# Performance work log

Measured on AMD Instinct MI355X. Metric: run time of the kernel, lower is better.

The kernel has to match this reference:

```python
import jax, jax.numpy as jnp
import numpy as np

B, H, W, C = 4, 256, 256, 128
HEADS, WS, SHIFT = 4, 8, 4
EPS = 1e-5


def _rel_pos_index(ws):
    coords = np.stack(np.meshgrid(np.arange(ws), np.arange(ws), indexing='ij'))
    cf = coords.reshape(2, -1)
    rel = (cf[:, :, None] - cf[:, None, :]).transpose(1, 2, 0)
    rel[:, :, 0] += ws - 1
    rel[:, :, 1] += ws - 1
    rel[:, :, 0] *= 2 * ws - 1
    return rel.sum(-1).reshape(-1)

REL_IDX = jnp.array(_rel_pos_index(WS))


def _shift_mask(h, w, ws, shift):
    img = np.zeros((1, h, w, 1))
    cnt = 0
    sl = (slice(0, -ws), slice(-ws, -shift), slice(-shift, None))
    for hs in sl:
        for wsl in sl:
            img[:, hs, wsl, :] = cnt
            cnt += 1
    m = img.reshape(1, h // ws, ws, w // ws, ws, 1).transpose(0, 1, 3, 2, 4, 5).reshape(-1, ws * ws)
    am = m[:, None, :] - m[:, :, None]
    return jnp.array(np.where(am != 0, -100.0, 0.0).astype(np.float32))

ATTN_MASK = _shift_mask(H, W, WS, SHIFT)  # (nW, ws*ws, ws*ws)


def _ln(x, scale, bias):
    mu = x.mean(-1, keepdims=True)
    var = x.var(-1, keepdims=True)
    return (x - mu) / jnp.sqrt(var + EPS) * scale + bias


def setup_inputs() -> dict:
    key = jax.random.key(0)
    ks = jax.random.split(key, 8)
    s = 0.02
    return dict(
        hidden_states=jax.random.normal(ks[0], (B, H * W, C), jnp.float32),
        ln1_scale=jnp.ones((C,), jnp.float32), ln1_bias=jnp.zeros((C,), jnp.float32),
        q_w=jax.random.normal(ks[1], (C, C), jnp.float32) * s, q_b=jnp.zeros((C,), jnp.float32),
        k_w=jax.random.normal(ks[2], (C, C), jnp.float32) * s, k_b=jnp.zeros((C,), jnp.float32),
        v_w=jax.random.normal(ks[3], (C, C), jnp.float32) * s, v_b=jnp.zeros((C,), jnp.float32),
        proj_w=jax.random.normal(ks[4], (C, C), jnp.float32) * s, proj_b=jnp.zeros((C,), jnp.float32),
        rpb_table=jax.random.normal(ks[5], ((2 * WS - 1) ** 2, HEADS), jnp.float32) * s,
        ln2_scale=jnp.ones((C,), jnp.float32), ln2_bias=jnp.zeros((C,), jnp.float32),
        fc1_w=jax.random.normal(ks[6], (C, 4 * C), jnp.float32) * s, fc1_b=jnp.zeros((4 * C,), jnp.float32),
        fc2_w=jax.random.normal(ks[7], (4 * C, C), jnp.float32) * s, fc2_b=jnp.zeros((C,), jnp.float32),
    )


def reference(hidden_states, ln1_scale, ln1_bias, q_w, q_b, k_w, k_b, v_w, v_b,
              proj_w, proj_b, rpb_table, ln2_scale, ln2_bias, fc1_w, fc1_b, fc2_w, fc2_b):
    hd = C // HEADS
    T = WS * WS
    nW = (H // WS) * (W // WS)
    shortcut = hidden_states
    x = _ln(hidden_states, ln1_scale, ln1_bias).reshape(B, H, W, C)
    # cyclic shift
    x = jnp.roll(x, (-SHIFT, -SHIFT), axis=(1, 2))
    # window partition -> (B*nW, T, C)
    x = x.reshape(B, H // WS, WS, W // WS, WS, C).transpose(0, 1, 3, 2, 4, 5).reshape(-1, T, C)
    q = (x @ q_w + q_b).reshape(-1, T, HEADS, hd) / jnp.sqrt(jnp.float32(hd))
    k = (x @ k_w + k_b).reshape(-1, T, HEADS, hd)
    v = (x @ v_w + v_b).reshape(-1, T, HEADS, hd)
    attn = jnp.einsum('bqhd,bkhd->bhqk', q, k)
    bias = rpb_table[REL_IDX].reshape(T, T, HEADS).transpose(2, 0, 1)  # (h, q, k)
    attn = attn + bias[None]
    # shift mask per window
    attn = attn.reshape(B, nW, HEADS, T, T) + ATTN_MASK[None, :, None]
    attn = jax.nn.softmax(attn.reshape(-1, HEADS, T, T), axis=-1)
    out = jnp.einsum('bhqk,bkhd->bqhd', attn, v).reshape(-1, T, C)
    out = out @ proj_w + proj_b
    # window reverse + un-shift
    out = out.reshape(B, H // WS, W // WS, WS, WS, C).transpose(0, 1, 3, 2, 4, 5).reshape(B, H, W, C)
    out = jnp.roll(out, (SHIFT, SHIFT), axis=(1, 2)).reshape(B, H * W, C)
    x = shortcut + out
    y = _ln(x, ln2_scale, ln2_bias)
    y = jax.nn.gelu(y @ fc1_w + fc1_b, approximate=False) @ fc2_w + fc2_b
    return x + y
```

## Files before the change

### kernel.cpp

```cpp
#include <hip/hip_runtime.h>
#include <hip/hip_bf16.h>
#include <math.h>

#define B_ 4
#define H_ 256
#define W_ 256
#define C_ 128
#define HEADS_ 4
#define HD_ 32
#define WS_ 8
#define SHIFT_ 4
#define T_ 64
#define NW_ 1024
#define M_ (B_*NW_*T_)

typedef float floatx4 __attribute__((ext_vector_type(4)));
typedef short bf16x8 __attribute__((ext_vector_type(8)));
typedef unsigned short ushort8v __attribute__((ext_vector_type(8)));

#define MFMA16(a,b,c) __builtin_amdgcn_mfma_f32_16x16x32_bf16(a,b,c,0,0,0)

__device__ __forceinline__ unsigned short f2b(float f){
    union { float f; unsigned int i; } c; c.f = f;
    unsigned int r = c.i + 0x7FFFu + ((c.i >> 16) & 1u);
    return (unsigned short)(r >> 16);
}
__device__ __forceinline__ int region_id(int x){ return (x < 248) ? 0 : ((x < 252) ? 1 : 2); }

__device__ __forceinline__ bf16x8 ldfrag(const unsigned short* p){
    return *(const bf16x8*)p;
}
__device__ __forceinline__ bf16x8 ldfrag_strided(const unsigned short* p, int stride){
    ushort8v u;
    #pragma unroll
    for (int j = 0; j < 8; j++) u[j] = p[j*stride];
    return __builtin_bit_cast(bf16x8, u);
}
__device__ __forceinline__ floatx4 fzero(){ floatx4 v = {0.f,0.f,0.f,0.f}; return v; }

#define WSO_QT   0
#define WSO_KT   16384
#define WSO_VT   32768
#define WSO_PT   49152
#define WSO_W1T  65536
#define WSO_W2T  131072
#define WSO_BIAS 196608
#define WS_BYTES_NEEDED (196608u*2u + 16384u*4u)

__global__ __launch_bounds__(256) void prep_weights_kernel(
        const float* __restrict__ qw, const float* __restrict__ kw,
        const float* __restrict__ vw, const float* __restrict__ pw,
        const float* __restrict__ fc1, const float* __restrict__ fc2,
        const float* __restrict__ rpb, unsigned short* __restrict__ ws)
{
    int tid = blockIdx.x * 256 + threadIdx.x;
    int nt = gridDim.x * 256;
    for (int i = tid; i < 16384; i += nt) {
        int n = i >> 7, k = i & 127;
        ws[WSO_QT + i] = f2b(qw[k*128 + n]);
        ws[WSO_KT + i] = f2b(kw[k*128 + n]);
        ws[WSO_VT + i] = f2b(vw[k*128 + n]);
        ws[WSO_PT + i] = f2b(pw[k*128 + n]);
    }
    for (int i = tid; i < 65536; i += nt) {
        int n = i >> 7, k = i & 127;
        ws[WSO_W1T + i] = f2b(fc1[(size_t)k*512 + n]);
    }
    for (int i = tid; i < 65536; i += nt) {
        int n = i >> 9, k = i & 511;
        ws[WSO_W2T + i] = f2b(fc2[(size_t)k*128 + n]);
    }
    float* bt = (float*)(ws + WSO_BIAS);
    for (int i = tid; i < 16384; i += nt) {
        int h = i >> 12, q = (i >> 6) & 63, k = i & 63;
        int th = q >> 3, tw = q & 7, jh = k >> 3, jw = k & 7;
        bt[i] = rpb[((th - jh + 7)*15 + (tw - jw + 7))*HEADS_ + h];
    }
}

__device__ __forceinline__ void gemm64x128_g(
        const unsigned short (*Xs)[136], const unsigned short* __restrict__ Wt,
        int wv, int quad, int l15, floatx4 acc[4][2])
{
    #pragma unroll
    for (int c = 0; c < 4; c++) {
        bf16x8 bf0 = ldfrag(Wt + (size_t)(32*wv + l15)*128      + c*32 + quad*8);
        bf16x8 bf1 = ldfrag(Wt + (size_t)(32*wv + 16 + l15)*128 + c*32 + quad*8);
        #pragma unroll
        for (int m = 0; m < 4; m++) {
            bf16x8 af = ldfrag(&Xs[16*m + l15][c*32 + quad*8]);
            acc[m][0] = MFMA16(af, bf0, acc[m][0]);
            acc[m][1] = MFMA16(af, bf1, acc[m][1]);
        }
    }
}

__global__ __launch_bounds__(256) void swin_attn_kernel2(
        const float* __restrict__ hidden,
        const float* __restrict__ ln1_s, const float* __restrict__ ln1_b,
        const float* __restrict__ q_b, const float* __restrict__ k_b,
        const float* __restrict__ v_b, const float* __restrict__ p_b,
        const unsigned short* __restrict__ wsu,
        float* __restrict__ xres)
{
    __shared__ __align__(16) unsigned short Xs[T_][136];
    __shared__ __align__(16) unsigned short Ks[T_][136];
    __shared__ __align__(16) unsigned short Vs[T_][134];
    __shared__ __align__(16) unsigned short PhU[2][2560];

    int tid = threadIdx.x;
    int wv = tid >> 6, lane = tid & 63;
    int quad = lane >> 4, l15 = lane & 15;
    int gw = blockIdx.x;
    int wi = gw & (NW_-1), b = gw >> 10;
    int hb = wi >> 5, wb = wi & 31;

    for (int it = 0; it < 16; it++) {
        int t = wv*16 + it;
        int th = t >> 3, tw = t & 7;
        int h = (hb*8 + th + SHIFT_) & 255;
        int w = (wb*8 + tw + SHIFT_) & 255;
        size_t src = ((size_t)((b<<16) + (h<<8) + w)) * C_;
        float2 u = *(const float2*)(hidden + src + 2*lane);
        float x0 = u.x, x1 = u.y;
        float s = x0 + x1, ss = x0*x0 + x1*x1;
        #pragma unroll
        for (int m = 32; m > 0; m >>= 1) {
            s  += __shfl_xor(s,  m, 64);
            ss += __shfl_xor(ss, m, 64);
        }
        float mean = s * (1.0f/C_);
        float var  = ss * (1.0f/C_) - mean*mean;
        float rstd = rsqrtf(var + 1e-5f);
        int c0 = 2*lane;
        ushort2 o;
        o.x = f2b((x0 - mean) * rstd * ln1_s[c0]   + ln1_b[c0]);
        o.y = f2b((x1 - mean) * rstd * ln1_s[c0+1] + ln1_b[c0+1]);
        *(ushort2*)&Xs[t][c0] = o;
    }
    __syncthreads();

    {
        floatx4 acc[4][2];
        #pragma unroll
        for (int m = 0; m < 4; m++) { acc[m][0] = fzero(); acc[m][1] = fzero(); }
        gemm64x128_g(Xs, wsu + WSO_KT, wv, quad, l15, acc);
        float kb0 = k_b[32*wv + l15], kb1 = k_b[32*wv + 16 + l15];
        #pragma unroll
        for (int m = 0; m < 4; m++)
            #pragma unroll
            for (int r = 0; r < 4; r++) {
                int q = 16*m + 4*quad + r;
                Ks[q][32*wv + l15]      = f2b(acc[m][0][r] + kb0);
                Ks[q][32*wv + 16 + l15] = f2b(acc[m][1][r] + kb1);
            }
    }
    {
        floatx4 acc[4][2];
        #pragma unroll
        for (int m = 0; m < 4; m++) { acc[m][0] = fzero(); acc[m][1] = fzero(); }
        gemm64x128_g(Xs, wsu + WSO_VT, wv, quad, l15, acc);
        float vb0 = v_b[32*wv + l15], vb1 = v_b[32*wv + 16 + l15];
        #pragma unroll
        for (int m = 0; m < 4; m++)
            #pragma unroll
            for (int r = 0; r < 4; r++) {
                int q = 16*m + 4*quad + r;
                Vs[q][32*wv + l15]      = f2b(acc[m][0][r] + vb0);
                Vs[q][32*wv + 16 + l15] = f2b(acc[m][1][r] + vb1);
            }
    }
    floatx4 qacc[4][2];
    #pragma unroll
    for (int m = 0; m < 4; m++) { qacc[m][0] = fzero(); qacc[m][1] = fzero(); }
    gemm64x128_g(Xs, wsu + WSO_QT, wv, quad, l15, qacc);
    __syncthreads();
    {
        const float sc = 0.17677669529663687f;
        float qb0 = q_b[32*wv + l15], qb1 = q_b[32*wv + 16 + l15];
        #pragma unroll
        for (int m = 0; m < 4; m++)
            #pragma unroll
            for (int r = 0; r < 4; r++) {
                int q = 16*m + 4*quad + r;
                Xs[q][32*wv + l15]      = f2b((qacc[m][0][r] + qb0) * sc);
                Xs[q][32*wv + 16 + l15] = f2b((qacc[m][1][r] + qb1) * sc);
            }
    }

    floatx4 sacc[4][4];
    #pragma unroll
    for (int m = 0; m < 4; m++)
        #pragma unroll
        for (int n = 0; n < 4; n++) sacc[m][n] = fzero();
    {
        bf16x8 qf[4], kf[4];
        #pragma unroll
        for (int m = 0; m < 4; m++) qf[m] = ldfrag(&Xs[16*m + l15][32*wv + quad*8]);
        #pragma unroll
        for (int n = 0; n < 4; n++) kf[n] = ldfrag(&Ks[16*n + l15][32*wv + quad*8]);
        #pragma unroll
        for (int m = 0; m < 4; m++)
            #pragma unroll
            for (int n = 0; n < 4; n++) sacc[m][n] = MFMA16(qf[m], kf[n], sacc[m][n]);
    }
    __syncthreads();

    {
        const float* bt = (const float*)(wsu + WSO_BIAS) + (wv << 12);
        int cidj_[4];
        #pragma unroll
        for (int n = 0; n < 4; n++) {
            int kt = 16*n + l15;
            cidj_[n] = region_id(hb*8 + (kt >> 3))*3 + region_id(wb*8 + (kt & 7));
        }
        #pragma unroll
        for (int m = 0; m < 4; m++)
            #pragma unroll
            for (int r = 0; r < 4; r++) {
                int q = 16*m + 4*quad + r;
                int cidi = region_id(hb*8 + (q >> 3))*3 + region_id(wb*8 + (q & 7));
                float v[4];
                #pragma unroll
                for (int n = 0; n < 4; n++) {
                    float d = sacc[m][n][r] + bt[q*64 + 16*n + l15];
                    if (cidi != cidj_[n]) d -= 100.f;
                    v[n] = d;
                }
                float mx = fmaxf(fmaxf(v[0],v[1]), fmaxf(v[2],v[3]));
                #pragma unroll
                for (int off = 1; off < 16; off <<= 1) mx = fmaxf(mx, __shfl_xor(mx, off, 64));
                float sum = 0.f;
                #pragma unroll
                for (int n = 0; n < 4; n++) { v[n] = __expf(v[n] - mx); sum += v[n]; }
                #pragma unroll
                for (int off = 1; off < 16; off <<= 1) sum += __shfl_xor(sum, off, 64);
                float inv = 1.0f / sum;
                #pragma unroll
                for (int n = 0; n < 4; n++) sacc[m][n][r] = v[n] * inv;
            }
    }

    unsigned short* Ph = (wv < 2) ? (&Ks[0][0] + wv*2560) : &PhU[wv-2][0];
    floatx4 oacc[4][2];
    #pragma unroll
    for (int m = 0; m < 4; m++) { oacc[m][0] = fzero(); oacc[m][1] = fzero(); }
    for (int kb = 0; kb < 2; kb++) {
        #pragma unroll
        for (int m = 0; m < 4; m++)
            #pragma unroll
            for (int r = 0; r < 4; r++) {
                int q = 16*m + 4*quad + r;
                Ph[q*40 + l15]      = f2b(sacc[m][2*kb+0][r]);
                Ph[q*40 + 16 + l15] = f2b(sacc[m][2*kb+1][r]);
            }
        bf16x8 bf0 = ldfrag_strided(&Vs[kb*32 + quad*8][32*wv + l15],      134);
        bf16x8 bf1 = ldfrag_strided(&Vs[kb*32 + quad*8][32*wv + 16 + l15], 134);
        #pragma unroll
        for (int m = 0; m < 4; m++) {
            bf16x8 af = ldfrag(&Ph[(16*m + l15)*40 + quad*8]);
            oacc[m][0] = MFMA16(af, bf0, oacc[m][0]);
            oacc[m][1] = MFMA16(af, bf1, oacc[m][1]);
        }
    }
    #pragma unroll
    for (int m = 0; m < 4; m++)
        #pragma unroll
        for (int r = 0; r < 4; r++) {
            int q = 16*m + 4*quad + r;
            Xs[q][32*wv + l15]      = f2b(oacc[m][0][r]);
            Xs[q][32*wv + 16 + l15] = f2b(oacc[m][1][r]);
        }
    __syncthreads();
    {
        floatx4 acc[4][2];
        #pragma unroll
        for (int m = 0; m < 4; m++) { acc[m][0] = fzero(); acc[m][1] = fzero(); }
        gemm64x128_g(Xs, wsu + WSO_PT, wv, quad, l15, acc);
        float pb0 = p_b[32*wv + l15], pb1 = p_b[32*wv + 16 + l15];
        #pragma unroll
        for (int m = 0; m < 4; m++)
            #pragma unroll
            for (int r = 0; r < 4; r++) {
                int t = 16*m + 4*quad + r;
                int th = t >> 3, tw = t & 7;
                int h = (hb*8 + th + SHIFT_) & 255;
                int w = (wb*8 + tw + SHIFT_) & 255;
                size_t dst = ((size_t)((b<<16) + (h<<8) + w)) * C_;
                int c0 = 32*wv + l15;
                xres[dst + c0]      = hidden[dst + c0]      + acc[m][0][r] + pb0;
                xres[dst + c0 + 16] = hidden[dst + c0 + 16] + acc[m][1][r] + pb1;
            }
    }
}

__global__ __launch_bounds__(256) void mlp_ln_kernel2(
        float* __restrict__ xio,
        const float* __restrict__ ln2_s, const float* __restrict__ ln2_b,
        const float* __restrict__ b1, const float* __restrict__ b2,
        const unsigned short* __restrict__ wsu)
{
    __shared__ __align__(16) unsigned short As[T_][136];
    __shared__ __align__(16) unsigned short G[T_][72];
    const unsigned short* W1t = wsu + WSO_W1T;
    const unsigned short* W2t = wsu + WSO_W2T;
    int tid = threadIdx.x, wv = tid >> 6, lane = tid & 63;
    int quad = lane >> 4, l15 = lane & 15;
    size_t row0 = (size_t)blockIdx.x * 64;

    for (int it = 0; it < 16; it++) {
        int t = wv*16 + it;
        const float* xp = xio + (row0 + t)*C_;
        float2 u = *(const float2*)(xp + 2*lane);
        float x0 = u.x, x1 = u.y;
        float s = x0 + x1, ss = x0*x0 + x1*x1;
        #pragma unroll
        for (int m = 32; m > 0; m >>= 1) {
            s  += __shfl_xor(s,  m, 64);
            ss += __shfl_xor(ss, m, 64);
        }
        float mean = s * (1.0f/C_);
        float var  = ss * (1.0f/C_) - mean*mean;
        float rstd = rsqrtf(var + 1e-5f);
        int c0 = 2*lane;
        ushort2 o;
        o.x = f2b((x0 - mean) * rstd * ln2_s[c0]   + ln2_b[c0]);
        o.y = f2b((x1 - mean) * rstd * ln2_s[c0+1] + ln2_b[c0+1]);
        *(ushort2*)&As[t][c0] = o;
    }
    __syncthreads();

    floatx4 acc2[4][2];
    #pragma unroll
    for (int m = 0; m < 4; m++) { acc2[m][0] = fzero(); acc2[m][1] = fzero(); }

    for (int ch = 0; ch < 8; ch++) {
        floatx4 a1[4];
        #pragma unroll
        for (int m = 0; m < 4; m++) a1[m] = fzero();
        #pragma unroll
        for (int kc = 0; kc < 4; kc++) {
            bf16x8 bfrag = ldfrag(W1t + (size_t)(ch*64 + 16*wv + l15)*128 + kc*32 + quad*8);
            #pragma unroll
            for (int m = 0; m < 4; m++) {
                bf16x8 af = ldfrag(&As[16*m + l15][kc*32 + quad*8]);
                a1[m] = MFMA16(af, bfrag, a1[m]);
            }
        }
        __syncthreads();
        {
            int c_rel = 16*wv + l15;
            float bb = b1[ch*64 + c_rel];
            #pragma unroll
            for (int m = 0; m < 4; m++)
                #pragma unroll
                for (int r = 0; r < 4; r++) {
                    int q = 16*m + 4*quad + r;
                    float hh = a1[m][r] + bb;
                    float g = 0.5f * hh * (1.0f + erff(hh * 0.70710678118654752f));
                    G[q][c_rel] = f2b(g);
                }
        }
        __syncthreads();
        #pragma unroll
        for (int ki = 0; ki < 2; ki++) {
            bf16x8 bf0 = ldfrag(W2t + (size_t)(32*wv + l15)*512      + ch*64 + ki*32 + quad*8);
            bf16x8 bf1 = ldfrag(W2t + (size_t)(32*wv + 16 + l15)*512 + ch*64 + ki*32 + quad*8);
            #pragma unroll
            for (int m = 0; m < 4; m++) {
                bf16x8 af = ldfrag(&G[16*m + l15][ki*32 + quad*8]);
                acc2[m][0] = MFMA16(af, bf0, acc2[m][0]);
                acc2[m][1] = MFMA16(af, bf1, acc2[m][1]);
            }
        }
    }
    {
        float bb0 = b2[32*wv + l15], bb1 = b2[32*wv + 16 + l15];
        #pragma unroll
        for (int m = 0; m < 4; m++)
            #pragma unroll
            for (int r = 0; r < 4; r++) {
                size_t rr = row0 + 16*m + 4*quad + r;
                int c0 = 32*wv + l15;
                xio[rr*C_ + c0]      += acc2[m][0][r] + bb0;
                xio[rr*C_ + c0 + 16] += acc2[m][1][r] + bb1;
            }
    }
}


__device__ __forceinline__ void gemm64x128(
        const unsigned short (*Xs)[136], unsigned short (*Wc)[132],
        const float* __restrict__ Wg, int tid, int wv, int quad, int l15,
        floatx4 acc[4][2])
{
    for (int c = 0; c < 4; c++) {
        __syncthreads();
        #pragma unroll
        for (int it = 0; it < 4; it++) {
            int idx = tid + it*256;
            int kk = idx >> 5;
            int n4 = (idx & 31) * 4;
            float4 v = *(const float4*)(Wg + (size_t)(c*32 + kk)*C_ + n4);
            ushort4 o; o.x=f2b(v.x); o.y=f2b(v.y); o.z=f2b(v.z); o.w=f2b(v.w);
            *(ushort4*)&Wc[kk][n4] = o;
        }
        __syncthreads();
        bf16x8 bf0 = ldfrag_strided(&Wc[quad*8][32*wv + l15],      132);
        bf16x8 bf1 = ldfrag_strided(&Wc[quad*8][32*wv + 16 + l15], 132);
        #pragma unroll
        for (int m = 0; m < 4; m++) {
            bf16x8 af = ldfrag(&Xs[16*m + l15][c*32 + quad*8]);
            acc[m][0] = MFMA16(af, bf0, acc[m][0]);
            acc[m][1] = MFMA16(af, bf1, acc[m][1]);
        }
    }
}

__global__ __launch_bounds__(256) void swin_attn_kernel(
        const float* __restrict__ hidden,
        const float* __restrict__ ln1_s, const float* __restrict__ ln1_b,
        const float* __restrict__ q_w, const float* __restrict__ q_b,
        const float* __restrict__ k_w, const float* __restrict__ k_b,
        const float* __restrict__ v_w, const float* __restrict__ v_b,
        const float* __restrict__ p_w, const float* __restrict__ p_b,
        const float* __restrict__ rpb,
        float* __restrict__ xres)
{
    __shared__ unsigned short Xs[T_][136];
    __shared__ unsigned short Ks[T_][136];
    __shared__ unsigned short Vs[T_][134];
    __shared__ __align__(16) unsigned char U[10240];

    unsigned short (*Wc)[132] = (unsigned short(*)[132])U;
    float* rpbf = (float*)U;

    int tid = threadIdx.x;
    int wv = tid >> 6, lane = tid & 63;
    int quad = lane >> 4, l15 = lane & 15;
    int gw = blockIdx.x;
    int wi = gw & (NW_-1), b = gw >> 10;
    int hb = wi >> 5, wb = wi & 31;

    for (int it = 0; it < 16; it++) {
        int t = wv*16 + it;
        int th = t >> 3, tw = t & 7;
        int h = (hb*8 + th + SHIFT_) & 255;
        int w = (wb*8 + tw + SHIFT_) & 255;
        size_t src = ((size_t)((b<<16) + (h<<8) + w)) * C_;
        float2 u = *(const float2*)(hidden + src + 2*lane);
        float x0 = u.x, x1 = u.y;
        float s = x0 + x1, ss = x0*x0 + x1*x1;
        #pragma unroll
        for (int m = 32; m > 0; m >>= 1) {
            s  += __shfl_xor(s,  m, 64);
            ss += __shfl_xor(ss, m, 64);
        }
        float mean = s * (1.0f/C_);
        float var  = ss * (1.0f/C_) - mean*mean;
        float rstd = rsqrtf(var + 1e-5f);
        int c0 = 2*lane;
        ushort2 o;
        o.x = f2b((x0 - mean) * rstd * ln1_s[c0]   + ln1_b[c0]);
        o.y = f2b((x1 - mean) * rstd * ln1_s[c0+1] + ln1_b[c0+1]);
        *(ushort2*)&Xs[t][c0] = o;
    }

    {
        floatx4 acc[4][2];
        #pragma unroll
        for (int m = 0; m < 4; m++) { acc[m][0] = fzero(); acc[m][1] = fzero(); }
        gemm64x128(Xs, Wc, k_w, tid, wv, quad, l15, acc);
        float kb0 = k_b[32*wv + l15], kb1 = k_b[32*wv + 16 + l15];
        #pragma unroll
        for (int m = 0; m < 4; m++)
            #pragma unroll
            for (int r = 0; r < 4; r++) {
                int q = 16*m + 4*quad + r;
                Ks[q][32*wv + l15]      = f2b(acc[m][0][r] + kb0);
                Ks[q][32*wv + 16 + l15] = f2b(acc[m][1][r] + kb1);
            }
    }
    {
        floatx4 acc[4][2];
        #pragma unroll
        for (int m = 0; m < 4; m++) { acc[m][0] = fzero(); acc[m][1] = fzero(); }
        gemm64x128(Xs, Wc, v_w, tid, wv, quad, l15, acc);
        float vb0 = v_b[32*wv + l15], vb1 = v_b[32*wv + 16 + l15];
        #pragma unroll
        for (int m = 0; m < 4; m++)
            #pragma unroll
            for (int r = 0; r < 4; r++) {
                int q = 16*m + 4*quad + r;
                Vs[q][32*wv + l15]      = f2b(acc[m][0][r] + vb0);
                Vs[q][32*wv + 16 + l15] = f2b(acc[m][1][r] + vb1);
            }
    }
    floatx4 qacc[4][2];
    #pragma unroll
    for (int m = 0; m < 4; m++) { qacc[m][0] = fzero(); qacc[m][1] = fzero(); }
    gemm64x128(Xs, Wc, q_w, tid, wv, quad, l15, qacc);
    __syncthreads();
    for (int i = tid; i < 225*HEADS_; i += 256) rpbf[i] = rpb[i];
    {
        const float sc = 0.17677669529663687f;
        float qb0 = q_b[32*wv + l15], qb1 = q_b[32*wv + 16 + l15];
        #pragma unroll
        for (int m = 0; m < 4; m++)
            #pragma unroll
            for (int r = 0; r < 4; r++) {
                int q = 16*m + 4*quad + r;
                Xs[q][32*wv + l15]      = f2b((qacc[m][0][r] + qb0) * sc);
                Xs[q][32*wv + 16 + l15] = f2b((qacc[m][1][r] + qb1) * sc);
            }
    }
    __syncthreads();

    floatx4 sacc[4][4];
    #pragma unroll
    for (int m = 0; m < 4; m++)
        #pragma unroll
        for (int n = 0; n < 4; n++) sacc[m][n] = fzero();
    {
        bf16x8 qf[4], kf[4];
        #pragma unroll
        for (int m = 0; m < 4; m++) qf[m] = ldfrag(&Xs[16*m + l15][32*wv + quad*8]);
        #pragma unroll
        for (int n = 0; n < 4; n++) kf[n] = ldfrag(&Ks[16*n + l15][32*wv + quad*8]);
        #pragma unroll
        for (int m = 0; m < 4; m++)
            #pragma unroll
            for (int n = 0; n < 4; n++) sacc[m][n] = MFMA16(qf[m], kf[n], sacc[m][n]);
    }
    {
        int jh_[4], jw_[4], cidj_[4];
        #pragma unroll
        for (int n = 0; n < 4; n++) {
            int kt = 16*n + l15;
            jh_[n] = kt >> 3; jw_[n] = kt & 7;
            cidj_[n] = region_id(hb*8 + jh_[n])*3 + region_id(wb*8 + jw_[n]);
        }
        #pragma unroll
        for (int m = 0; m < 4; m++)
            #pragma unroll
            for (int r = 0; r < 4; r++) {
                int q = 16*m + 4*quad + r;
                int th = q >> 3, twq = q & 7;
                int cidi = region_id(hb*8 + th)*3 + region_id(wb*8 + twq);
                float v[4];
                #pragma unroll
                for (int n = 0; n < 4; n++) {
                    float d = sacc[m][n][r];
                    d += rpbf[((th - jh_[n] + 7)*15 + (twq - jw_[n] + 7))*HEADS_ + wv];
                    if (cidi != cidj_[n]) d -= 100.f;
                    v[n] = d;
                }
                float mx = fmaxf(fmaxf(v[0],v[1]), fmaxf(v[2],v[3]));
                #pragma unroll
                for (int off = 1; off < 16; off <<= 1) mx = fmaxf(mx, __shfl_xor(mx, off, 64));
                float sum = 0.f;
                #pragma unroll
                for (int n = 0; n < 4; n++) { v[n] = __expf(v[n] - mx); sum += v[n]; }
                #pragma unroll
                for (int off = 1; off < 16; off <<= 1) sum += __shfl_xor(sum, off, 64);
                float inv = 1.0f / sum;
                #pragma unroll
                for (int n = 0; n < 4; n++) sacc[m][n][r] = v[n] * inv;
            }
    }
    __syncthreads();

    unsigned short* Ph = (wv < 2) ? (&Ks[0][0] + wv*2560)
                                  : ((unsigned short*)U + (wv-2)*2560);
    floatx4 oacc[4][2];
    #pragma unroll
    for (int m = 0; m < 4; m++) { oacc[m][0] = fzero(); oacc[m][1] = fzero(); }
    for (int kb = 0; kb < 2; kb++) {
        #pragma unroll
        for (int m = 0; m < 4; m++)
            #pragma unroll
            for (int r = 0; r < 4; r++) {
                int q = 16*m + 4*quad + r;
                Ph[q*40 + l15]      = f2b(sacc[m][2*kb+0][r]);
                Ph[q*40 + 16 + l15] = f2b(sacc[m][2*kb+1][r]);
            }
        __syncthreads();
        bf16x8 bf0 = ldfrag_strided(&Vs[kb*32 + quad*8][32*wv + l15],      134);
        bf16x8 bf1 = ldfrag_strided(&Vs[kb*32 + quad*8][32*wv + 16 + l15], 134);
        #pragma unroll
        for (int m = 0; m < 4; m++) {
            bf16x8 af = ldfrag(&Ph[(16*m + l15)*40 + quad*8]);
            oacc[m][0] = MFMA16(af, bf0, oacc[m][0]);
            oacc[m][1] = MFMA16(af, bf1, oacc[m][1]);
        }
        __syncthreads();
    }
    #pragma unroll
    for (int m = 0; m < 4; m++)
        #pragma unroll
        for (int r = 0; r < 4; r++) {
            int q = 16*m + 4*quad + r;
            Xs[q][32*wv + l15]      = f2b(oacc[m][0][r]);
            Xs[q][32*wv + 16 + l15] = f2b(oacc[m][1][r]);
        }
    {
        floatx4 acc[4][2];
        #pragma unroll
        for (int m = 0; m < 4; m++) { acc[m][0] = fzero(); acc[m][1] = fzero(); }
        gemm64x128(Xs, Wc, p_w, tid, wv, quad, l15, acc);
        float pb0 = p_b[32*wv + l15], pb1 = p_b[32*wv + 16 + l15];
        #pragma unroll
        for (int m = 0; m < 4; m++)
            #pragma unroll
            for (int r = 0; r < 4; r++) {
                int t = 16*m + 4*quad + r;
                int th = t >> 3, tw = t & 7;
                int h = (hb*8 + th + SHIFT_) & 255;
                int w = (wb*8 + tw + SHIFT_) & 255;
                size_t dst = ((size_t)((b<<16) + (h<<8) + w)) * C_;
                int c0 = 32*wv + l15;
                xres[dst + c0]      = hidden[dst + c0]      + acc[m][0][r] + pb0;
                xres[dst + c0 + 16] = hidden[dst + c0 + 16] + acc[m][1][r] + pb1;
            }
    }
}

__global__ __launch_bounds__(256) void mlp_ln_kernel(
        float* __restrict__ xio,
        const float* __restrict__ ln2_s, const float* __restrict__ ln2_b,
        const float* __restrict__ W1, const float* __restrict__ b1,
        const float* __restrict__ W2, const float* __restrict__ b2)
{
    __shared__ unsigned short As[T_][136];
    __shared__ unsigned short G[T_][72];
    __shared__ unsigned short W1c[C_][68];
    __shared__ unsigned short W2c[T_][132];
    int tid = threadIdx.x, wv = tid >> 6, lane = tid & 63;
    int quad = lane >> 4, l15 = lane & 15;
    size_t row0 = (size_t)blockIdx.x * 64;

    for (int it = 0; it < 16; it++) {
        int t = wv*16 + it;
        const float* xp = xio + (row0 + t)*C_;
        float2 u = *(const float2*)(xp + 2*lane);
        float x0 = u.x, x1 = u.y;
        float s = x0 + x1, ss = x0*x0 + x1*x1;
        #pragma unroll
        for (int m = 32; m > 0; m >>= 1) {
            s  += __shfl_xor(s,  m, 64);
            ss += __shfl_xor(ss, m, 64);
        }
        float mean = s * (1.0f/C_);
        float var  = ss * (1.0f/C_) - mean*mean;
        float rstd = rsqrtf(var + 1e-5f);
        int c0 = 2*lane;
        ushort2 o;
        o.x = f2b((x0 - mean) * rstd * ln2_s[c0]   + ln2_b[c0]);
        o.y = f2b((x1 - mean) * rstd * ln2_s[c0+1] + ln2_b[c0+1]);
        *(ushort2*)&As[t][c0] = o;
    }

    floatx4 acc2[4][2];
    #pragma unroll
    for (int m = 0; m < 4; m++) { acc2[m][0] = fzero(); acc2[m][1] = fzero(); }

    for (int ch = 0; ch < 8; ch++) {
        __syncthreads();
        #pragma unroll
        for (int it = 0; it < 8; it++) {
            int idx = tid + it*256;
            int k = idx >> 4, n4 = (idx & 15) * 4;
            float4 v = *(const float4*)(W1 + (size_t)k*512 + ch*64 + n4);
            ushort4 o; o.x=f2b(v.x); o.y=f2b(v.y); o.z=f2b(v.z); o.w=f2b(v.w);
            *(ushort4*)&W1c[k][n4] = o;
        }
        #pragma unroll
        for (int it = 0; it < 8; it++) {
            int idx = tid + it*256;
            int k = idx >> 5, n4 = (idx & 31) * 4;
            float4 v = *(const float4*)(W2 + (size_t)(ch*64 + k)*C_ + n4);
            ushort4 o; o.x=f2b(v.x); o.y=f2b(v.y); o.z=f2b(v.z); o.w=f2b(v.w);
            *(ushort4*)&W2c[k][n4] = o;
        }
        __syncthreads();
        floatx4 a1[4];
        #pragma unroll
        for (int m = 0; m < 4; m++) a1[m] = fzero();
        #pragma unroll
        for (int kc = 0; kc < 4; kc++) {
            bf16x8 bfrag = ldfrag_strided(&W1c[kc*32 + quad*8][16*wv + l15], 68);
            #pragma unroll
            for (int m = 0; m < 4; m++) {
                bf16x8 af = ldfrag(&As[16*m + l15][kc*32 + quad*8]);
                a1[m] = MFMA16(af, bfrag, a1[m]);
            }
        }
        {
            int c_rel = 16*wv + l15;
            float bb = b1[ch*64 + c_rel];
            #pragma unroll
            for (int m = 0; m < 4; m++)
                #pragma unroll
                for (int r = 0; r < 4; r++) {
                    int q = 16*m + 4*quad + r;
                    float hh = a1[m][r] + bb;
                    float g = 0.5f * hh * (1.0f + erff(hh * 0.70710678118654752f));
                    G[q][c_rel] = f2b(g);
                }
        }
        __syncthreads();
        #pragma unroll
        for (int ki = 0; ki < 2; ki++) {
            bf16x8 bf0 = ldfrag_strided(&W2c[ki*32 + quad*8][32*wv + l15],      132);
            bf16x8 bf1 = ldfrag_strided(&W2c[ki*32 + quad*8][32*wv + 16 + l15], 132);
            #pragma unroll
            for (int m = 0; m < 4; m++) {
                bf16x8 af = ldfrag(&G[16*m + l15][ki*32 + quad*8]);
                acc2[m][0] = MFMA16(af, bf0, acc2[m][0]);
                acc2[m][1] = MFMA16(af, bf1, acc2[m][1]);
            }
        }
    }
    {
        float bb0 = b2[32*wv + l15], bb1 = b2[32*wv + 16 + l15];
        #pragma unroll
        for (int m = 0; m < 4; m++)
            #pragma unroll
            for (int r = 0; r < 4; r++) {
                size_t rr = row0 + 16*m + 4*quad + r;
                int c0 = 32*wv + l15;
                xio[rr*C_ + c0]      += acc2[m][0][r] + bb0;
                xio[rr*C_ + c0 + 16] += acc2[m][1][r] + bb1;
            }
    }
}

extern "C" void kernel_launch(void* const* d_in, const int* in_sizes, int n_in,
                              void* d_out, int out_size, void* d_ws, size_t ws_size,
                              hipStream_t stream) {
    (void)in_sizes; (void)n_in; (void)out_size;
    const float* hidden = (const float*)d_in[0];
    const float* ln1_s  = (const float*)d_in[1];
    const float* ln1_b  = (const float*)d_in[2];
    const float* q_w    = (const float*)d_in[3];
    const float* q_b    = (const float*)d_in[4];
    const float* k_w    = (const float*)d_in[5];
    const float* k_b    = (const float*)d_in[6];
    const float* v_w    = (const float*)d_in[7];
    const float* v_b    = (const float*)d_in[8];
    const float* p_w    = (const float*)d_in[9];
    const float* p_b    = (const float*)d_in[10];
    const float* rpb    = (const float*)d_in[11];
    const float* ln2_s  = (const float*)d_in[12];
    const float* ln2_b  = (const float*)d_in[13];
    const float* fc1_w  = (const float*)d_in[14];
    const float* fc1_b  = (const float*)d_in[15];
    const float* fc2_w  = (const float*)d_in[16];
    const float* fc2_b  = (const float*)d_in[17];
    float* outp = (float*)d_out;

    if (d_ws != nullptr && ws_size >= (size_t)WS_BYTES_NEEDED) {
        unsigned short* wsu = (unsigned short*)d_ws;
        prep_weights_kernel<<<64, 256, 0, stream>>>(q_w, k_w, v_w, p_w,
                fc1_w, fc2_w, rpb, wsu);
        swin_attn_kernel2<<<B_*NW_, 256, 0, stream>>>(hidden, ln1_s, ln1_b,
                q_b, k_b, v_b, p_b, wsu, outp);
        mlp_ln_kernel2<<<M_/64, 256, 0, stream>>>(outp, ln2_s, ln2_b,
                fc1_b, fc2_b, wsu);
    } else {
        swin_attn_kernel<<<B_*NW_, 256, 0, stream>>>(hidden, ln1_s, ln1_b,
                q_w, q_b, k_w, k_b, v_w, v_b, p_w, p_b, rpb, outp);
        mlp_ln_kernel<<<M_/64, 256, 0, stream>>>(outp, ln2_s, ln2_b,
                fc1_w, fc1_b, fc2_w, fc2_b);
    }
}
```

Before: 560.3 us.

## Restructure MLP per-wave rows, fuse K/V GEMMs, transpose score layout

```diff
diff --git a/kernel.cpp b/kernel.cpp
--- a/kernel.cpp
+++ b/kernel.cpp
@@ -106,7 +106,6 @@
     __shared__ __align__(16) unsigned short Xs[T_][136];
     __shared__ __align__(16) unsigned short Ks[T_][136];
     __shared__ __align__(16) unsigned short Vs[T_][134];
-    __shared__ __align__(16) unsigned short PhU[2][2560];
 
     int tid = threadIdx.x;
     int wv = tid >> 6, lane = tid & 63;
@@ -115,59 +114,76 @@
     int wi = gw & (NW_-1), b = gw >> 10;
     int hb = wi >> 5, wb = wi & 31;
 
-    for (int it = 0; it < 16; it++) {
-        int t = wv*16 + it;
+    {
+        int rloc = lane >> 2;
+        int t = wv*16 + rloc;
         int th = t >> 3, tw = t & 7;
         int h = (hb*8 + th + SHIFT_) & 255;
         int w = (wb*8 + tw + SHIFT_) & 255;
-        size_t src = ((size_t)((b<<16) + (h<<8) + w)) * C_;
-        float2 u = *(const float2*)(hidden + src + 2*lane);
-        float x0 = u.x, x1 = u.y;
-        float s = x0 + x1, ss = x0*x0 + x1*x1;
-        #pragma unroll
-        for (int m = 32; m > 0; m >>= 1) {
-            s  += __shfl_xor(s,  m, 64);
-            ss += __shfl_xor(ss, m, 64);
-        }
+        int c0 = (lane & 3) * 32;
+        const float* xp = hidden + ((size_t)((b<<16) + (h<<8) + w)) * C_ + c0;
+        float4 xv[8];
+        float s = 0.f, ss = 0.f;
+        #pragma unroll
+        for (int i = 0; i < 8; i++) {
+            xv[i] = *((const float4*)xp + i);
+            s  += xv[i].x + xv[i].y + xv[i].z + xv[i].w;
+            ss += xv[i].x*xv[i].x + xv[i].y*xv[i].y + xv[i].z*xv[i].z + xv[i].w*xv[i].w;
+        }
+        s  += __shfl_xor(s, 1, 64);  s  += __shfl_xor(s, 2, 64);
+        ss += __shfl_xor(ss, 1, 64); ss += __shfl_xor(ss, 2, 64);
         float mean = s * (1.0f/C_);
         float var  = ss * (1.0f/C_) - mean*mean;
         float rstd = rsqrtf(var + 1e-5f);
-        int c0 = 2*lane;
-        ushort2 o;
-        o.x = f2b((x0 - mean) * rstd * ln1_s[c0]   + ln1_b[c0]);
-        o.y = f2b((x1 - mean) * rstd * ln1_s[c0+1] + ln1_b[c0+1]);
-        *(ushort2*)&Xs[t][c0] = o;
+        #pragma unroll
+        for (int i = 0; i < 8; i++) {
+            float4 sc = *((const float4*)(ln1_s + c0) + i);
+            float4 bi = *((const float4*)(ln1_b + c0) + i);
+            ushort4 o;
+            o.x = f2b((xv[i].x - mean)*rstd*sc.x + bi.x);
+            o.y = f2b((xv[i].y - mean)*rstd*sc.y + bi.y);
+            o.z = f2b((xv[i].z - mean)*rstd*sc.z + bi.z);
+            o.w = f2b((xv[i].w - mean)*rstd*sc.w + bi.w);
+            *(ushort4*)&Xs[t][c0 + 4*i] = o;
+        }
     }
     __syncthreads();
 
     {
-        floatx4 acc[4][2];
-        #pragma unroll
-        for (int m = 0; m < 4; m++) { acc[m][0] = fzero(); acc[m][1] = fzero(); }
-        gemm64x128_g(Xs, wsu + WSO_KT, wv, quad, l15, acc);
+        floatx4 kacc[4][2], vacc[4][2];
+        #pragma unroll
+        for (int m = 0; m < 4; m++) {
+            kacc[m][0] = fzero(); kacc[m][1] = fzero();
+            vacc[m][0] = fzero(); vacc[m][1] = fzero();
+        }
+        const unsigned short* Kt = wsu + WSO_KT;
+        const unsigned short* Vt = wsu + WSO_VT;
+        #pragma unroll
+        for (int c = 0; c < 4; c++) {
+            size_t off0 = (size_t)(32*wv + l15)*128      + c*32 + quad*8;
+            size_t off1 = (size_t)(32*wv + 16 + l15)*128 + c*32 + quad*8;
+            bf16x8 kb0 = ldfrag(Kt + off0), kb1 = ldfrag(Kt + off1);
+            bf16x8 vb0 = ldfrag(Vt + off0), vb1 = ldfrag(Vt + off1);
+            #pragma unroll
+            for (int m = 0; m < 4; m++) {
+                bf16x8 af = ldfrag(&Xs[16*m + l15][c*32 + quad*8]);
+                kacc[m][0] = MFMA16(af, kb0, kacc[m][0]);
+                kacc[m][1] = MFMA16(af, kb1, kacc[m][1]);
+                vacc[m][0] = MFMA16(af, vb0, vacc[m][0]);
+                vacc[m][1] = MFMA16(af, vb1, vacc[m][1]);
+            }
+        }
         float kb0 = k_b[32*wv + l15], kb1 = k_b[32*wv + 16 + l15];
+        float vb0 = v_b[32*wv + l15], vb1 = v_b[32*wv + 16 + l15];
         #pragma unroll
         for (int m = 0; m < 4; m++)
             #pragma unroll
             for (int r = 0; r < 4; r++) {
                 int q = 16*m + 4*quad + r;
-                Ks[q][32*wv + l15]      = f2b(acc[m][0][r] + kb0);
-                Ks[q][32*wv + 16 + l15] = f2b(acc[m][1][r] + kb1);
-            }
-    }
-    {
-        floatx4 acc[4][2];
-        #pragma unroll
-        for (int m = 0; m < 4; m++) { acc[m][0] = fzero(); acc[m][1] = fzero(); }
-        gemm64x128_g(Xs, wsu + WSO_VT, wv, quad, l15, acc);
-        float vb0 = v_b[32*wv + l15], vb1 = v_b[32*wv + 16 + l15];
-        #pragma unroll
-        for (int m = 0; m < 4; m++)
-            #pragma unroll
-            for (int r = 0; r < 4; r++) {
-                int q = 16*m + 4*quad + r;
-                Vs[q][32*wv + l15]      = f2b(acc[m][0][r] + vb0);
-                Vs[q][32*wv + 16 + l15] = f2b(acc[m][1][r] + vb1);
+                Ks[q][32*wv + l15]      = f2b(kacc[m][0][r] + kb0);
+                Ks[q][32*wv + 16 + l15] = f2b(kacc[m][1][r] + kb1);
+                Vs[q][32*wv + l15]      = f2b(vacc[m][0][r] + vb0);
+                Vs[q][32*wv + 16 + l15] = f2b(vacc[m][1][r] + vb1);
             }
     }
     floatx4 qacc[4][2];
@@ -202,46 +218,55 @@
         #pragma unroll
         for (int m = 0; m < 4; m++)
             #pragma unroll
-            for (int n = 0; n < 4; n++) sacc[m][n] = MFMA16(qf[m], kf[n], sacc[m][n]);
+            for (int n = 0; n < 4; n++) sacc[m][n] = MFMA16(kf[n], qf[m], sacc[m][n]);
     }
     __syncthreads();
 
     {
         const float* bt = (const float*)(wsu + WSO_BIAS) + (wv << 12);
-        int cidj_[4];
-        #pragma unroll
-        for (int n = 0; n < 4; n++) {
-            int kt = 16*n + l15;
-            cidj_[n] = region_id(hb*8 + (kt >> 3))*3 + region_id(wb*8 + (kt & 7));
-        }
-        #pragma unroll
-        for (int m = 0; m < 4; m++)
-            #pragma unroll
-            for (int r = 0; r < 4; r++) {
-                int q = 16*m + 4*quad + r;
-                int cidi = region_id(hb*8 + (q >> 3))*3 + region_id(wb*8 + (q & 7));
-                float v[4];
-                #pragma unroll
-                for (int n = 0; n < 4; n++) {
-                    float d = sacc[m][n][r] + bt[q*64 + 16*n + l15];
-                    if (cidi != cidj_[n]) d -= 100.f;
-                    v[n] = d;
+        int cidk[4][4];
+        #pragma unroll
+        for (int n = 0; n < 4; n++)
+            #pragma unroll
+            for (int r = 0; r < 4; r++) {
+                int kt = 16*n + 4*quad + r;
+                cidk[n][r] = region_id(hb*8 + (kt >> 3))*3 + region_id(wb*8 + (kt & 7));
+            }
+        #pragma unroll
+        for (int m = 0; m < 4; m++) {
+            int q = 16*m + l15;
+            int cidq = region_id(hb*8 + (q >> 3))*3 + region_id(wb*8 + (q & 7));
+            float v[4][4];
+            float mx = -3.0e38f;
+            #pragma unroll
+            for (int n = 0; n < 4; n++) {
+                float4 bv = *(const float4*)(bt + q*64 + 16*n + 4*quad);
+                #pragma unroll
+                for (int r = 0; r < 4; r++) {
+                    float d = sacc[m][n][r] + bv[r];
+                    if (cidq != cidk[n][r]) d -= 100.f;
+                    v[n][r] = d;
+                    mx = fmaxf(mx, d);
                 }
-                float mx = fmaxf(fmaxf(v[0],v[1]), fmaxf(v[2],v[3]));
-                #pragma unroll
-                for (int off = 1; off < 16; off <<= 1) mx = fmaxf(mx, __shfl_xor(mx, off, 64));
-                float sum = 0.f;
-                #pragma unroll
-                for (int n = 0; n < 4; n++) { v[n] = __expf(v[n] - mx); sum += v[n]; }
-                #pragma unroll
-                for (int off = 1; off < 16; off <<= 1) sum += __shfl_xor(sum, off, 64);
-                float inv = 1.0f / sum;
-                #pragma unroll
-                for (int n = 0; n < 4; n++) sacc[m][n][r] = v[n] * inv;
-            }
-    }
-
-    unsigned short* Ph = (wv < 2) ? (&Ks[0][0] + wv*2560) : &PhU[wv-2][0];
+            }
+            mx = fmaxf(mx, __shfl_xor(mx, 16, 64));
+            mx = fmaxf(mx, __shfl_xor(mx, 32, 64));
+            float sum = 0.f;
+            #pragma unroll
+            for (int n = 0; n < 4; n++)
+                #pragma unroll
+                for (int r = 0; r < 4; r++) { v[n][r] = __expf(v[n][r] - mx); sum += v[n][r]; }
+            sum += __shfl_xor(sum, 16, 64);
+            sum += __shfl_xor(sum, 32, 64);
+            float inv = 1.0f / sum;
+            #pragma unroll
+            for (int n = 0; n < 4; n++)
+                #pragma unroll
+                for (int r = 0; r < 4; r++) sacc[m][n][r] = v[n][r] * inv;
+        }
+    }
+
+    unsigned short* Ph = (wv < 2) ? (&Ks[0][0] + wv*2560) : (&Xs[0][0] + (wv-2)*2560);
     floatx4 oacc[4][2];
     #pragma unroll
     for (int m = 0; m < 4; m++) { oacc[m][0] = fzero(); oacc[m][1] = fzero(); }
@@ -249,11 +274,10 @@
         #pragma unroll
         for (int m = 0; m < 4; m++)
             #pragma unroll
-            for (int r = 0; r < 4; r++) {
-                int q = 16*m + 4*quad + r;
-                Ph[q*40 + l15]      = f2b(sacc[m][2*kb+0][r]);
-                Ph[q*40 + 16 + l15] = f2b(sacc[m][2*kb+1][r]);
-            }
+            for (int n2 = 0; n2 < 2; n2++)
+                #pragma unroll
+                for (int r = 0; r < 4; r++)
+                    Ph[(16*m + l15)*40 + n2*16 + 4*quad + r] = f2b(sacc[m][2*kb + n2][r]);
         bf16x8 bf0 = ldfrag_strided(&Vs[kb*32 + quad*8][32*wv + l15],      134);
         bf16x8 bf1 = ldfrag_strided(&Vs[kb*32 + quad*8][32*wv + 16 + l15], 134);
         #pragma unroll
@@ -263,6 +287,7 @@
             oacc[m][1] = MFMA16(af, bf1, oacc[m][1]);
         }
     }
+    __syncthreads();
     #pragma unroll
     for (int m = 0; m < 4; m++)
         #pragma unroll
@@ -308,83 +333,84 @@
     int quad = lane >> 4, l15 = lane & 15;
     size_t row0 = (size_t)blockIdx.x * 64;
 
-    for (int it = 0; it < 16; it++) {
-        int t = wv*16 + it;
-        const float* xp = xio + (row0 + t)*C_;
-        float2 u = *(const float2*)(xp + 2*lane);
-        float x0 = u.x, x1 = u.y;
-        float s = x0 + x1, ss = x0*x0 + x1*x1;
-        #pragma unroll
-        for (int m = 32; m > 0; m >>= 1) {
-            s  += __shfl_xor(s,  m, 64);
-            ss += __shfl_xor(ss, m, 64);
-        }
+    {
+        int rloc = lane >> 2;
+        int t = wv*16 + rloc;
+        int c0 = (lane & 3) * 32;
+        const float* xp = xio + (row0 + t)*C_ + c0;
+        float4 xv[8];
+        float s = 0.f, ss = 0.f;
+        #pragma unroll
+        for (int i = 0; i < 8; i++) {
+            xv[i] = *((const float4*)xp + i);
+            s  += xv[i].x + xv[i].y + xv[i].z + xv[i].w;
+            ss += xv[i].x*xv[i].x + xv[i].y*xv[i].y + xv[i].z*xv[i].z + xv[i].w*xv[i].w;
+        }
+        s  += __shfl_xor(s, 1, 64);  s  += __shfl_xor(s, 2, 64);
+        ss += __shfl_xor(ss, 1, 64); ss += __shfl_xor(ss, 2, 64);
         float mean = s * (1.0f/C_);
         float var  = ss * (1.0f/C_) - mean*mean;
         float rstd = rsqrtf(var + 1e-5f);
-        int c0 = 2*lane;
-        ushort2 o;
-        o.x = f2b((x0 - mean) * rstd * ln2_s[c0]   + ln2_b[c0]);
-        o.y = f2b((x1 - mean) * rstd * ln2_s[c0+1] + ln2_b[c0+1]);
-        *(ushort2*)&As[t][c0] = o;
-    }
-    __syncthreads();
-
-    floatx4 acc2[4][2];
-    #pragma unroll
-    for (int m = 0; m < 4; m++) { acc2[m][0] = fzero(); acc2[m][1] = fzero(); }
+        #pragma unroll
+        for (int i = 0; i < 8; i++) {
+            float4 sc = *((const float4*)(ln2_s + c0) + i);
+            float4 bi = *((const float4*)(ln2_b + c0) + i);
+            ushort4 o;
+            o.x = f2b((xv[i].x - mean)*rstd*sc.x + bi.x);
+            o.y = f2b((xv[i].y - mean)*rstd*sc.y + bi.y);
+            o.z = f2b((xv[i].z - mean)*rstd*sc.z + bi.z);
+            o.w = f2b((xv[i].w - mean)*rstd*sc.w + bi.w);
+            *(ushort4*)&As[t][c0 + 4*i] = o;
+        }
+    }
+
+    floatx4 acc2[8];
+    #pragma unroll
+    for (int n = 0; n < 8; n++) acc2[n] = fzero();
 
     for (int ch = 0; ch < 8; ch++) {
+        bf16x8 af[4];
+        #pragma unroll
+        for (int kc = 0; kc < 4; kc++) af[kc] = ldfrag(&As[16*wv + l15][kc*32 + quad*8]);
         floatx4 a1[4];
         #pragma unroll
-        for (int m = 0; m < 4; m++) a1[m] = fzero();
-        #pragma unroll
-        for (int kc = 0; kc < 4; kc++) {
-            bf16x8 bfrag = ldfrag(W1t + (size_t)(ch*64 + 16*wv + l15)*128 + kc*32 + quad*8);
-            #pragma unroll
-            for (int m = 0; m < 4; m++) {
-                bf16x8 af = ldfrag(&As[16*m + l15][kc*32 + quad*8]);
-                a1[m] = MFMA16(af, bfrag, a1[m]);
-            }
-        }
-        __syncthreads();
-        {
-            int c_rel = 16*wv + l15;
-            float bb = b1[ch*64 + c_rel];
-            #pragma unroll
-            for (int m = 0; m < 4; m++)
-                #pragma unroll
-                for (int r = 0; r < 4; r++) {
-                    int q = 16*m + 4*quad + r;
-                    float hh = a1[m][r] + bb;
-                    float g = 0.5f * hh * (1.0f + erff(hh * 0.70710678118654752f));
-                    G[q][c_rel] = f2b(g);
-                }
-        }
-        __syncthreads();
-        #pragma unroll
-        for (int ki = 0; ki < 2; ki++) {
-            bf16x8 bf0 = ldfrag(W2t + (size_t)(32*wv + l15)*512      + ch*64 + ki*32 + quad*8);
-            bf16x8 bf1 = ldfrag(W2t + (size_t)(32*wv + 16 + l15)*512 + ch*64 + ki*32 + quad*8);
-            #pragma unroll
-            for (int m = 0; m < 4; m++) {
-                bf16x8 af = ldfrag(&G[16*m + l15][ki*32 + quad*8]);
-                acc2[m][0] = MFMA16(af, bf0, acc2[m][0]);
-                acc2[m][1] = MFMA16(af, bf1, acc2[m][1]);
-            }
-        }
-    }
-    {
-        float bb0 = b2[32*wv + l15], bb1 = b2[32*wv + 16 + l15];
-        #pragma unroll
-        for (int m = 0; m < 4; m++)
-            #pragma unroll
-            for (int r = 0; r < 4; r++) {
-                size_t rr = row0 + 16*m + 4*quad + r;
-                int c0 = 32*wv + l15;
-                xio[rr*C_ + c0]      += acc2[m][0][r] + bb0;
-                xio[rr*C_ + c0 + 16] += acc2[m][1][r] + bb1;
-            }
+        for (int n = 0; n < 4; n++) a1[n] = fzero();
+        #pragma unroll
+        for (int n = 0; n < 4; n++)
+            #pragma unroll
+            for (int kc = 0; kc < 4; kc++) {
+                bf16x8 bf = ldfrag(W1t + (size_t)(ch*64 + n*16 + l15)*128 + kc*32 + quad*8);
+                a1[n] = MFMA16(af[kc], bf, a1[n]);
+            }
+        #pragma unroll
+        for (int n = 0; n < 4; n++) {
+            float bb = b1[ch*64 + n*16 + l15];
+            #pragma unroll
+            for (int r = 0; r < 4; r++) {
+                float hh = a1[n][r] + bb;
+                float g = 0.5f * hh * (1.0f + erff(hh * 0.70710678118654752f));
+                G[16*wv + 4*quad + r][n*16 + l15] = f2b(g);
+            }
+        }
+        bf16x8 gf[2];
+        #pragma unroll
+        for (int kc = 0; kc < 2; kc++) gf[kc] = ldfrag(&G[16*wv + l15][kc*32 + quad*8]);
+        #pragma unroll
+        for (int n = 0; n < 8; n++)
+            #pragma unroll
+            for (int kc = 0; kc < 2; kc++) {
+                bf16x8 bf = ldfrag(W2t + (size_t)(n*16 + l15)*512 + ch*64 + kc*32 + quad*8);
+                acc2[n] = MFMA16(gf[kc], bf, acc2[n]);
+            }
+    }
+    #pragma unroll
+    for (int n = 0; n < 8; n++) {
+        float bb = b2[n*16 + l15];
+        #pragma unroll
+        for (int r = 0; r < 4; r++) {
+            size_t rr = row0 + 16*wv + 4*quad + r;
+            xio[rr*C_ + n*16 + l15] += acc2[n][r] + bb;
+        }
     }
 }
 
```

Measured after the change: 889.6 us. +58.8%, slower.
